# Kernel tuning notes

Measured on AMD Instinct MI355X. Metric: run time of the kernel, lower is better.

The kernel has to match this reference:

```python
import jax, jax.numpy as jnp
import numpy as np

N = 50000      # nodes
E = 800000     # edges (avg degree 16)
IN = 128       # in_channels
OUT = 64       # out_channels
HID = 2 * OUT  # 128, hidden width of conv1
EPS = 1e-5     # BatchNorm eps


def _edge_norm(edge_index):
    # PyG ChebConv with sym normalization, lambda_max=2: L_hat = -D^{-1/2} A D^{-1/2}
    src, dst = edge_index[0], edge_index[1]
    deg = jax.ops.segment_sum(jnp.ones((E,), jnp.float32), src, num_segments=N)
    dinv = jnp.where(deg > 0, jax.lax.rsqrt(jnp.maximum(deg, 1.0)), 0.0)
    return -dinv[src] * dinv[dst]


def _cheb(x, src, dst, norm, W0, W1, b):
    # K=2 Chebyshev conv: Tx0 = x, Tx1 = L_hat x (sparse propagate)
    tx1 = jax.ops.segment_sum(x[src] * norm[:, None], dst, num_segments=N)
    return x @ W0 + tx1 @ W1 + b


def setup_inputs() -> dict:
    key = jax.random.key(0)
    ks = jax.random.split(key, 14)
    g = lambda k, shp, fan: jax.random.normal(k, shp, jnp.float32) / np.sqrt(fan)
    return {
        "x": jax.random.normal(ks[0], (N, IN), jnp.float32),
        "edge_index": jax.random.randint(ks[1], (2, E), 0, N, dtype=jnp.int32),
        "W1_0": g(ks[2], (IN, HID), IN),
        "W1_1": g(ks[3], (IN, HID), IN),
        "b1": jnp.zeros((HID,), jnp.float32),
        "gamma": jnp.ones((HID,), jnp.float32),
        "beta": jnp.zeros((HID,), jnp.float32),
        "Wmu_0": g(ks[4], (HID, OUT), HID),
        "Wmu_1": g(ks[5], (HID, OUT), HID),
        "b_mu": jnp.zeros((OUT,), jnp.float32),
        "Wls_0": g(ks[6], (HID, OUT), HID),
        "Wls_1": g(ks[7], (HID, OUT), HID),
        "b_ls": jnp.zeros((OUT,), jnp.float32),
    }


def reference(x, edge_index, W1_0, W1_1, b1, gamma, beta,
              Wmu_0, Wmu_1, b_mu, Wls_0, Wls_1, b_ls):
    src, dst = edge_index[0], edge_index[1]
    norm = _edge_norm(edge_index)
    h = _cheb(x, src, dst, norm, W1_0, W1_1, b1)         # [N, HID]
    # BatchNorm1d (training mode: batch statistics over nodes)
    mean = jnp.mean(h, axis=0)
    var = jnp.var(h, axis=0)
    h = (h - mean) * jax.lax.rsqrt(var + EPS) * gamma + beta
    h = jax.nn.relu(h)
    mu = _cheb(h, src, dst, norm, Wmu_0, Wmu_1, b_mu)    # [N, OUT]
    logstd = _cheb(h, src, dst, norm, Wls_0, Wls_1, b_ls)
    return (mu, logstd)
```

## Files before the change

### kernel.cpp

```cpp
#include <hip/hip_runtime.h>
#include <cstddef>
#include <cstdint>

static constexpr int IN_C  = 128;
static constexpr float BN_EPS = 1e-5f;
static constexpr int OUT_C = 64;

static constexpr int CS_C = 32;
static constexpr int CS_R = 8;
static constexpr int CS_RANGE = 6250;

using bf16x8 = __attribute__((ext_vector_type(8))) short;
using f32x4  = __attribute__((ext_vector_type(4))) float;

__device__ __forceinline__ ushort f2bf(float f) {
    uint u = __float_as_uint(f);
    u += 0x7fffu + ((u >> 16) & 1u);
    return (ushort)(u >> 16);
}
__device__ __forceinline__ uint pack2(float a, float b) {
    return (uint)f2bf(a) | ((uint)f2bf(b) << 16);
}
__device__ __forceinline__ float bf_lo(uint v) { return __uint_as_float(v << 16); }
__device__ __forceinline__ float bf_hi(uint v) { return __uint_as_float(v & 0xffff0000u); }

__global__ __launch_bounds__(1024) void hist_k(
    const int* __restrict__ src, const int* __restrict__ dst,
    int* __restrict__ hsrc_part, int* __restrict__ hdst_part,
    int N, int E, int chunk, int range) {
    __shared__ int hs_[CS_RANGE];
    __shared__ int hd_[CS_RANGE];
    int c = blockIdx.x & (CS_C - 1);
    int r = blockIdx.x / CS_C;
    int base = r * range;
    int hi = min(base + range, N);
    int rsz = hi - base;
    for (int j = threadIdx.x; j < rsz; j += 1024) { hs_[j] = 0; hd_[j] = 0; }
    __syncthreads();
    int e0 = c * chunk, e1 = min(e0 + chunk, E);
    for (int i = e0 + threadIdx.x; i < e1; i += 1024) {
        int s = src[i];
        if (s >= base && s < hi) atomicAdd(&hs_[s - base], 1);
        int t = dst[i];
        if (t >= base && t < hi) atomicAdd(&hd_[t - base], 1);
    }
    __syncthreads();
    for (int j = threadIdx.x; j < rsz; j += 1024) {
        hsrc_part[(size_t)c * N + base + j] = hs_[j];
        hdst_part[(size_t)c * N + base + j] = hd_[j];
    }
}

__global__ void reduce_hist_k(const int* __restrict__ hsrc_part,
                              const int* __restrict__ hdst_part,
                              float* __restrict__ dinv, int* __restrict__ cnt_dst, int N) {
    int v = blockIdx.x * 256 + threadIdx.x;
    if (v >= N) return;
    int a = 0, b = 0;
    for (int c = 0; c < CS_C; ++c) {
        a += hsrc_part[(size_t)c * N + v];
        b += hdst_part[(size_t)c * N + v];
    }
    dinv[v] = (a > 0) ? rsqrtf((float)a) : 0.f;
    cnt_dst[v] = b;
}

__global__ void scan_reduce_k(const int* __restrict__ cnt, int* __restrict__ bsum, int n) {
    __shared__ int sw[16];
    int tid = threadIdx.x;
    int i0 = blockIdx.x * 4096 + tid * 4;
    int t = 0;
    if (i0 + 3 < n) {
        int4 c = *(const int4*)(cnt + i0);
        t = c.x + c.y + c.z + c.w;
    } else {
        #pragma unroll
        for (int j = 0; j < 4; ++j) if (i0 + j < n) t += cnt[i0 + j];
    }
    #pragma unroll
    for (int off = 1; off < 64; off <<= 1) t += __shfl_xor(t, off, 64);
    if ((tid & 63) == 0) sw[tid >> 6] = t;
    __syncthreads();
    if (tid == 0) {
        int a = 0;
        #pragma unroll
        for (int w = 0; w < 16; ++w) a += sw[w];
        bsum[blockIdx.x] = a;
    }
}

__global__ void scan_bsum_k(int* __restrict__ bsum, int nb) {
    int lane = threadIdx.x;
    int v = (lane < nb) ? bsum[lane] : 0;
    int s = v;
    #pragma unroll
    for (int off = 1; off < 64; off <<= 1) {
        int t = __shfl_up(s, off, 64);
        if (lane >= off) s += t;
    }
    if (lane < nb) bsum[lane] = s - v;
}

__global__ void scan_phase3_k(const int* __restrict__ cnt, const int* __restrict__ bsum,
                              int* __restrict__ row_ptr, int n) {
    __shared__ int sm_w[16];
    __shared__ int sm_excl[16];
    int tid = threadIdx.x;
    int lane = tid & 63, wid = tid >> 6;
    int base = blockIdx.x * 4096;
    int running = bsum[blockIdx.x];
    if (blockIdx.x == 0 && tid == 0) row_ptr[0] = 0;
    int i0 = base + tid * 4;
    int c0 = (i0     < n) ? cnt[i0]     : 0;
    int c1 = (i0 + 1 < n) ? cnt[i0 + 1] : 0;
    int c2 = (i0 + 2 < n) ? cnt[i0 + 2] : 0;
    int c3 = (i0 + 3 < n) ? cnt[i0 + 3] : 0;
    int tsum = c0 + c1 + c2 + c3;
    int s = tsum;
    #pragma unroll
    for (int off = 1; off < 64; off <<= 1) {
        int t = __shfl_up(s, off, 64);
        if (lane >= off) s += t;
    }
    if (lane == 63) sm_w[wid] = s;
    __syncthreads();
    if (tid == 0) {
        int acc = 0;
        #pragma unroll
        for (int w = 0; w < 16; ++w) { sm_excl[w] = acc; acc += sm_w[w]; }
    }
    __syncthreads();
    int excl = running + sm_excl[wid] + (s - tsum);
    if (i0     < n) row_ptr[i0 + 1] = excl + c0;
    if (i0 + 1 < n) row_ptr[i0 + 2] = excl + c0 + c1;
    if (i0 + 2 < n) row_ptr[i0 + 3] = excl + c0 + c1 + c2;
    if (i0 + 3 < n) row_ptr[i0 + 4] = excl + tsum;
}

__global__ void chunk_off_k(int* __restrict__ hdst_part, const int* __restrict__ row_ptr, int N) {
    int v = blockIdx.x * 256 + threadIdx.x;
    if (v >= N) return;
    int run = row_ptr[v];
    for (int c = 0; c < CS_C; ++c) {
        size_t idx = (size_t)c * N + v;
        int t = hdst_part[idx];
        hdst_part[idx] = run;
        run += t;
    }
}

__global__ __launch_bounds__(1024) void scatter_k(
    const int* __restrict__ src, const int* __restrict__ dst,
    const int* __restrict__ off, int* __restrict__ col,
    int N, int E, int chunk, int range) {
    __shared__ int cur[CS_RANGE];
    int c = blockIdx.x & (CS_C - 1);
    int r = blockIdx.x / CS_C;
    int base = r * range;
    int hi = min(base + range, N);
    int rsz = hi - base;
    for (int j = threadIdx.x; j < rsz; j += 1024)
        cur[j] = off[(size_t)c * N + base + j];
    __syncthreads();
    int e0 = c * chunk, e1 = min(e0 + chunk, E);
    for (int i = e0 + threadIdx.x; i < e1; i += 1024) {
        int t = dst[i];
        if (t >= base && t < hi) {
            int pos = atomicAdd(&cur[t - base], 1);
            col[pos] = src[i];
        }
    }
}

__global__ void convert_x_k(const float* __restrict__ in, const float* __restrict__ dinv,
                            ushort* __restrict__ xb, ushort* __restrict__ xsb, int n64) {
    int i = blockIdx.x * blockDim.x + threadIdx.x;
    if (i >= n64) return;
    int row = i >> 6;
    float d = dinv[row];
    float2 v = ((const float2*)in)[i];
    ((uint*)xb)[i] = pack2(v.x, v.y);
    ((uint*)xsb)[i] = pack2(v.x * d, v.y * d);
}

__global__ void prep_weights_k(const float* __restrict__ W1_0, const float* __restrict__ W1_1,
                               const float* __restrict__ b1,
                               const float* __restrict__ Wmu_0, const float* __restrict__ Wmu_1,
                               const float* __restrict__ b_mu,
                               const float* __restrict__ Wls_0, const float* __restrict__ Wls_1,
                               const float* __restrict__ b_ls,
                               ushort* __restrict__ Wt1, ushort* __restrict__ Wt2,
                               float* __restrict__ bias1, float* __restrict__ bias2) {
    int idx = blockIdx.x * blockDim.x + threadIdx.x;
    int which = idx >> 15;
    int c = (idx >> 8) & 127;
    int k = idx & 255;
    if (which == 0) {
        float v = (k < 128) ? W1_0[k * 128 + c] : W1_1[(k - 128) * 128 + c];
        Wt1[c * 256 + k] = f2bf(v);
        if (k == 0) bias1[c] = b1[c];
    } else {
        float v;
        if (c < 64) v = (k < 128) ? Wmu_0[k * 64 + c] : Wmu_1[(k - 128) * 64 + c];
        else        v = (k < 128) ? Wls_0[k * 64 + (c - 64)] : Wls_1[(k - 128) * 64 + (c - 64)];
        Wt2[c * 256 + k] = f2bf(v);
        if (k == 0) bias2[c] = (c < 64) ? b_mu[c] : b_ls[c - 64];
    }
}

#define ACC8(V)                                         \
    acc[0] += bf_lo((V).x); acc[1] += bf_hi((V).x);     \
    acc[2] += bf_lo((V).y); acc[3] += bf_hi((V).y);     \
    acc[4] += bf_lo((V).z); acc[5] += bf_hi((V).z);     \
    acc[6] += bf_lo((V).w); acc[7] += bf_hi((V).w);

__global__ __launch_bounds__(256) void propagate4_k(
    const uint4* __restrict__ xs, uint4* __restrict__ out,
    const int* __restrict__ row_ptr, const int* __restrict__ col,
    const float* __restrict__ dinv, int n) {
    int wid = (blockIdx.x * 256 + threadIdx.x) >> 6;
    if (wid >= n) return;
    int lane = threadIdx.x & 63;
    int g = lane >> 4, li = lane & 15;
    int s = row_ptr[wid], e = row_ptr[wid + 1];
    float acc[8];
    #pragma unroll
    for (int k = 0; k < 8; ++k) acc[k] = 0.f;
    int i = s + g;
    for (; i + 12 < e; i += 16) {
        int c0 = col[i];
        int c1 = col[i + 4];
        int c2 = col[i + 8];
        int c3 = col[i + 12];
        uint4 v0 = xs[(size_t)c0 * 16 + li];
        uint4 v1 = xs[(size_t)c1 * 16 + li];
        uint4 v2 = xs[(size_t)c2 * 16 + li];
        uint4 v3 = xs[(size_t)c3 * 16 + li];
        ACC8(v0); ACC8(v1); ACC8(v2); ACC8(v3);
    }
    for (; i < e; i += 4) {
        int c0 = col[i];
        uint4 v0 = xs[(size_t)c0 * 16 + li];
        ACC8(v0);
    }
    #pragma unroll
    for (int k = 0; k < 8; ++k) {
        acc[k] += __shfl_xor(acc[k], 16, 64);
        acc[k] += __shfl_xor(acc[k], 32, 64);
    }
    if (g == 0) {
        float sc = -dinv[wid];
        uint4 o;
        o.x = pack2(acc[0] * sc, acc[1] * sc);
        o.y = pack2(acc[2] * sc, acc[3] * sc);
        o.z = pack2(acc[4] * sc, acc[5] * sc);
        o.w = pack2(acc[6] * sc, acc[7] * sc);
        out[(size_t)wid * 16 + li] = o;
    }
}

template <int MODE>
__global__ __launch_bounds__(256) void gemm_mfma_k(
    const ushort* __restrict__ A0, const ushort* __restrict__ A1,
    const ushort* __restrict__ Wt, const float* __restrict__ bias,
    ushort* __restrict__ Cb, float* __restrict__ Cmu, float* __restrict__ Cls, int n) {
    __shared__ ushort sA[64][32];
    __shared__ ushort sW[128][32];

    int tid = threadIdx.x;
    int block_row = blockIdx.x * 64;
    int wave = tid >> 6, lane = tid & 63;
    int m_local = wave * 16 + (lane & 15);
    int quad = lane >> 4;

    f32x4 acc[8];
    #pragma unroll
    for (int t = 0; t < 8; ++t) acc[t] = (f32x4){0.f, 0.f, 0.f, 0.f};

    for (int k0 = 0; k0 < 256; k0 += 32) {
        {
            int row = tid >> 2, koff = (tid & 3) * 8;
            int grow = block_row + row;
            int kc = k0 + koff;
            uint4 v = make_uint4(0, 0, 0, 0);
            if (grow < n) {
                const ushort* srcp = (kc < 128) ? (A0 + (size_t)grow * 128 + kc)
                                                : (A1 + (size_t)grow * 128 + (kc - 128));
                v = *(const uint4*)srcp;
            }
            *(uint4*)&sA[row][koff] = v;
        }
        #pragma unroll
        for (int i = tid; i < 512; i += 256) {
            int c = i >> 2, koff = (i & 3) * 8;
            *(uint4*)&sW[c][koff] = *(const uint4*)(Wt + (size_t)c * 256 + k0 + koff);
        }
        __syncthreads();
        bf16x8 af = *(const bf16x8*)&sA[m_local][quad * 8];
        #pragma unroll
        for (int t = 0; t < 8; ++t) {
            bf16x8 bfr = *(const bf16x8*)&sW[t * 16 + (lane & 15)][quad * 8];
            acc[t] = __builtin_amdgcn_mfma_f32_16x16x32_bf16(af, bfr, acc[t], 0, 0, 0);
        }
        __syncthreads();
    }

    int col_base = lane & 15;
    int row_l = wave * 16 + quad * 4;
    #pragma unroll
    for (int t = 0; t < 8; ++t) {
        int col = t * 16 + col_base;
        float b = bias[col];
        #pragma unroll
        for (int r = 0; r < 4; ++r) {
            int grow = block_row + row_l + r;
            if (grow < n) {
                float v = acc[t][r] + b;
                if (MODE == 0) {
                    Cb[(size_t)grow * 128 + col] = f2bf(v);
                } else {
                    if (col < 64) Cmu[(size_t)grow * 64 + col] = v;
                    else          Cls[(size_t)grow * 64 + (col - 64)] = v;
                }
            }
        }
    }
}

__global__ __launch_bounds__(256) void bn_stats_k(const ushort* __restrict__ hb,
                                                  float* __restrict__ stats, int n) {
    __shared__ float sm[1024];
    int tid = threadIdx.x;
    int p = tid & 63;
    int rw = tid >> 6;
    float s0 = 0.f, q0 = 0.f, s1 = 0.f, q1 = 0.f;
    for (int r = blockIdx.x * 4 + rw; r < n; r += gridDim.x * 4) {
        uint v = ((const uint*)hb)[(size_t)r * 64 + p];
        float f0 = bf_lo(v), f1 = bf_hi(v);
        s0 += f0; q0 += f0 * f0;
        s1 += f1; q1 += f1 * f1;
    }
    sm[tid] = s0; sm[256 + tid] = q0; sm[512 + tid] = s1; sm[768 + tid] = q1;
    __syncthreads();
    if (tid < 64) {
        #pragma unroll
        for (int q = 0; q < 4; ++q) {
            float v = sm[q * 256 + tid] + sm[q * 256 + tid + 64] +
                      sm[q * 256 + tid + 128] + sm[q * 256 + tid + 192];
            int col = 2 * tid + (q >> 1);
            atomicAdd(&stats[col + ((q & 1) ? 128 : 0)], v);
        }
    }
}

__global__ void bn_finalize_k(const float* __restrict__ stats, const float* __restrict__ gamma,
                              const float* __restrict__ beta, float* __restrict__ p, float inv_n) {
    int c = threadIdx.x;
    float mean = stats[c] * inv_n;
    float var = stats[128 + c] * inv_n - mean * mean;
    float sc = gamma[c] * rsqrtf(var + BN_EPS);
    p[c] = sc;
    p[128 + c] = beta[c] - mean * sc;
}

__global__ void bn_apply_relu_bf_k(ushort* __restrict__ hb, ushort* __restrict__ hsb,
                                   const float* __restrict__ p, const float* __restrict__ dinv,
                                   int n64) {
    int i = blockIdx.x * blockDim.x + threadIdx.x;
    if (i >= n64) return;
    int c2 = (i & 63) * 2;
    int row = i >> 6;
    uint v = ((uint*)hb)[i];
    float f0 = fmaxf(bf_lo(v) * p[c2]     + p[128 + c2],     0.f);
    float f1 = fmaxf(bf_hi(v) * p[c2 + 1] + p[128 + c2 + 1], 0.f);
    ((uint*)hb)[i] = pack2(f0, f1);
    float d = dinv[row];
    ((uint*)hsb)[i] = pack2(f0 * d, f1 * d);
}

extern "C" void kernel_launch(void* const* d_in, const int* in_sizes, int n_in,
                              void* d_out, int out_size, void* d_ws, size_t ws_size,
                              hipStream_t stream) {
    const float* x = (const float*)d_in[0];
    const int* edge_index = (const int*)d_in[1];
    const float* W1_0 = (const float*)d_in[2];
    const float* W1_1 = (const float*)d_in[3];
    const float* b1 = (const float*)d_in[4];
    const float* gamma = (const float*)d_in[5];
    const float* beta = (const float*)d_in[6];
    const float* Wmu_0 = (const float*)d_in[7];
    const float* Wmu_1 = (const float*)d_in[8];
    const float* b_mu = (const float*)d_in[9];
    const float* Wls_0 = (const float*)d_in[10];
    const float* Wls_1 = (const float*)d_in[11];
    const float* b_ls = (const float*)d_in[12];

    const int N = in_sizes[0] / IN_C;
    const int E = in_sizes[1] / 2;
    const int* src = edge_index;
    const int* dst = edge_index + E;

    char* w = (char*)d_ws;
    auto alloc = [&](size_t bytes) {
        char* p = w;
        w += (bytes + 15) & ~(size_t)15;
        return p;
    };
    float* stats = (float*)alloc(256 * 4);
    size_t zero_bytes = (size_t)(w - (char*)stats);
    int* row_ptr = (int*)alloc((size_t)(N + 1) * 4);
    int* bsum    = (int*)alloc(64 * 4);
    float* dinv  = (float*)alloc((size_t)N * 4);
    int* cnt_dst = (int*)alloc((size_t)N * 4);
    int* col     = (int*)alloc((size_t)E * 4);
    int* hsrc_part = (int*)alloc((size_t)CS_C * N * 4);
    int* hdst_part = (int*)alloc((size_t)CS_C * N * 4);
    float* bnp   = (float*)alloc(256 * 4);
    ushort* x_bf  = (ushort*)alloc((size_t)N * 128 * 2);
    ushort* xs_bf = (ushort*)alloc((size_t)N * 128 * 2);
    ushort* xp_bf = (ushort*)alloc((size_t)N * 128 * 2);
    ushort* h_bf  = (ushort*)alloc((size_t)N * 128 * 2);
    ushort* Wt1   = (ushort*)alloc(128 * 256 * 2);
    ushort* Wt2   = (ushort*)alloc(128 * 256 * 2);
    float* bias1  = (float*)alloc(128 * 4);
    float* bias2  = (float*)alloc(128 * 4);

    ushort* hs_bf = xs_bf;
    ushort* hp_bf = xp_bf;

    float* out_mu = (float*)d_out;
    float* out_ls = out_mu + (size_t)N * OUT_C;

    hipMemsetAsync(stats, 0, zero_bytes, stream);

    int chunk = (E + CS_C - 1) / CS_C;
    int range = (N + CS_R - 1) / CS_R;
    int NB = (N + 4095) / 4096;

    hist_k<<<CS_R * CS_C, 1024, 0, stream>>>(src, dst, hsrc_part, hdst_part, N, E, chunk, range);
    reduce_hist_k<<<(N + 255) / 256, 256, 0, stream>>>(hsrc_part, hdst_part, dinv, cnt_dst, N);

    scan_reduce_k<<<NB, 1024, 0, stream>>>(cnt_dst, bsum, N);
    scan_bsum_k<<<1, 64, 0, stream>>>(bsum, NB);
    scan_phase3_k<<<NB, 1024, 0, stream>>>(cnt_dst, bsum, row_ptr, N);

    chunk_off_k<<<(N + 255) / 256, 256, 0, stream>>>(hdst_part, row_ptr, N);
    scatter_k<<<CS_R * CS_C, 1024, 0, stream>>>(src, dst, hdst_part, col, N, E, chunk, range);

    convert_x_k<<<(N * 64 + 255) / 256, 256, 0, stream>>>(x, dinv, x_bf, xs_bf, N * 64);
    prep_weights_k<<<256, 256, 0, stream>>>(W1_0, W1_1, b1, Wmu_0, Wmu_1, b_mu,
                                            Wls_0, Wls_1, b_ls, Wt1, Wt2, bias1, bias2);

    int pb = (N + 3) / 4;
    propagate4_k<<<pb, 256, 0, stream>>>((const uint4*)xs_bf, (uint4*)xp_bf,
                                         row_ptr, col, dinv, N);

    int gb = (N + 63) / 64;
    gemm_mfma_k<0><<<gb, 256, 0, stream>>>(x_bf, xp_bf, Wt1, bias1, h_bf, nullptr, nullptr, N);

    bn_stats_k<<<256, 256, 0, stream>>>(h_bf, stats, N);
    bn_finalize_k<<<1, 128, 0, stream>>>(stats, gamma, beta, bnp, 1.f / (float)N);
    bn_apply_relu_bf_k<<<(N * 64 + 255) / 256, 256, 0, stream>>>(h_bf, hs_bf, bnp, dinv, N * 64);

    propagate4_k<<<pb, 256, 0, stream>>>((const uint4*)hs_bf, (uint4*)hp_bf,
                                         row_ptr, col, dinv, N);

    gemm_mfma_k<1><<<gb, 256, 0, stream>>>(h_bf, hp_bf, Wt2, bias2, nullptr, out_mu, out_ls, N);
}
```

Measured before the change: 310.2 us.

## Fuse preprocessing kernels, drop memset and bn finalize, widen GEMM tile

Several small launches are merged. Histogram reduction is combined with the block-sum step, and the scan's final phase is combined with the per-chunk offset computation, which now uses int4 accesses. Input conversion is merged with weight prep, and BN finalize moves into the apply kernel. The stats memset is replaced by a zeroing write inside count_k, and each GEMM block now covers 128 rows with two accumulator sets. This removes roughly six launches and their gaps, but each phase3 block sums bsum serially, and the larger GEMM tile raises register use and halves the block count.

```diff
diff --git a/kernel.cpp b/kernel.cpp
--- a/kernel.cpp
+++ b/kernel.cpp
@@ -51,35 +51,32 @@
     }
 }
 
-__global__ void reduce_hist_k(const int* __restrict__ hsrc_part,
-                              const int* __restrict__ hdst_part,
-                              float* __restrict__ dinv, int* __restrict__ cnt_dst, int N) {
-    int v = blockIdx.x * 256 + threadIdx.x;
-    if (v >= N) return;
-    int a = 0, b = 0;
-    for (int c = 0; c < CS_C; ++c) {
-        a += hsrc_part[(size_t)c * N + v];
-        b += hdst_part[(size_t)c * N + v];
-    }
-    dinv[v] = (a > 0) ? rsqrtf((float)a) : 0.f;
-    cnt_dst[v] = b;
-}
-
-__global__ void scan_reduce_k(const int* __restrict__ cnt, int* __restrict__ bsum, int n) {
+__global__ __launch_bounds__(1024) void count_k(
+    const int* __restrict__ hsrc_part, const int* __restrict__ hdst_part,
+    float* __restrict__ dinv, int* __restrict__ cnt_dst,
+    int* __restrict__ bsum, float* __restrict__ stats, int N) {
     __shared__ int sw[16];
     int tid = threadIdx.x;
-    int i0 = blockIdx.x * 4096 + tid * 4;
-    int t = 0;
-    if (i0 + 3 < n) {
-        int4 c = *(const int4*)(cnt + i0);
-        t = c.x + c.y + c.z + c.w;
-    } else {
-        #pragma unroll
-        for (int j = 0; j < 4; ++j) if (i0 + j < n) t += cnt[i0 + j];
-    }
-    #pragma unroll
-    for (int off = 1; off < 64; off <<= 1) t += __shfl_xor(t, off, 64);
-    if ((tid & 63) == 0) sw[tid >> 6] = t;
+    if (blockIdx.x == 0 && tid < 256) stats[tid] = 0.f;
+    int base = blockIdx.x * 4096;
+    int tsum = 0;
+    #pragma unroll
+    for (int j = 0; j < 4; ++j) {
+        int v = base + j * 1024 + tid;
+        if (v < N) {
+            int a = 0, b = 0;
+            for (int c = 0; c < CS_C; ++c) {
+                a += hsrc_part[(size_t)c * N + v];
+                b += hdst_part[(size_t)c * N + v];
+            }
+            dinv[v] = (a > 0) ? rsqrtf((float)a) : 0.f;
+            cnt_dst[v] = b;
+            tsum += b;
+        }
+    }
+    #pragma unroll
+    for (int off = 1; off < 64; off <<= 1) tsum += __shfl_xor(tsum, off, 64);
+    if ((tid & 63) == 0) sw[tid >> 6] = tsum;
     __syncthreads();
     if (tid == 0) {
         int a = 0;
@@ -89,27 +86,21 @@
     }
 }
 
-__global__ void scan_bsum_k(int* __restrict__ bsum, int nb) {
-    int lane = threadIdx.x;
-    int v = (lane < nb) ? bsum[lane] : 0;
-    int s = v;
-    #pragma unroll
-    for (int off = 1; off < 64; off <<= 1) {
-        int t = __shfl_up(s, off, 64);
-        if (lane >= off) s += t;
-    }
-    if (lane < nb) bsum[lane] = s - v;
-}
-
-__global__ void scan_phase3_k(const int* __restrict__ cnt, const int* __restrict__ bsum,
-                              int* __restrict__ row_ptr, int n) {
+__global__ __launch_bounds__(1024) void phase3_k(
+    const int* __restrict__ cnt, const int* __restrict__ bsum,
+    int* __restrict__ row_ptr, int* __restrict__ hdst_part, int n, int nb) {
     __shared__ int sm_w[16];
     __shared__ int sm_excl[16];
+    __shared__ int sm_base;
     int tid = threadIdx.x;
     int lane = tid & 63, wid = tid >> 6;
     int base = blockIdx.x * 4096;
-    int running = bsum[blockIdx.x];
-    if (blockIdx.x == 0 && tid == 0) row_ptr[0] = 0;
+    if (tid == 0) {
+        int run = 0;
+        for (int b = 0; b < (int)blockIdx.x; ++b) run += bsum[b];
+        sm_base = run;
+        if (blockIdx.x == 0) row_ptr[0] = 0;
+    }
     int i0 = base + tid * 4;
     int c0 = (i0     < n) ? cnt[i0]     : 0;
     int c1 = (i0 + 1 < n) ? cnt[i0 + 1] : 0;
@@ -130,22 +121,25 @@
         for (int w = 0; w < 16; ++w) { sm_excl[w] = acc; acc += sm_w[w]; }
     }
     __syncthreads();
-    int excl = running + sm_excl[wid] + (s - tsum);
-    if (i0     < n) row_ptr[i0 + 1] = excl + c0;
-    if (i0 + 1 < n) row_ptr[i0 + 2] = excl + c0 + c1;
-    if (i0 + 2 < n) row_ptr[i0 + 3] = excl + c0 + c1 + c2;
+    int excl = sm_base + sm_excl[wid] + (s - tsum);
+    int st0 = excl, st1 = excl + c0, st2 = st1 + c1, st3 = st2 + c2;
+    if (i0     < n) row_ptr[i0 + 1] = st1;
+    if (i0 + 1 < n) row_ptr[i0 + 2] = st2;
+    if (i0 + 2 < n) row_ptr[i0 + 3] = st3;
     if (i0 + 3 < n) row_ptr[i0 + 4] = excl + tsum;
-}
-
-__global__ void chunk_off_k(int* __restrict__ hdst_part, const int* __restrict__ row_ptr, int N) {
-    int v = blockIdx.x * 256 + threadIdx.x;
-    if (v >= N) return;
-    int run = row_ptr[v];
+    int r0 = st0, r1 = st1, r2 = st2, r3 = st3;
     for (int c = 0; c < CS_C; ++c) {
-        size_t idx = (size_t)c * N + v;
-        int t = hdst_part[idx];
-        hdst_part[idx] = run;
-        run += t;
+        size_t idx = (size_t)c * n + i0;
+        if (i0 + 3 < n) {
+            int4 t = *(const int4*)(hdst_part + idx);
+            int4 o = make_int4(r0, r1, r2, r3);
+            *(int4*)(hdst_part + idx) = o;
+            r0 += t.x; r1 += t.y; r2 += t.z; r3 += t.w;
+        } else {
+            if (i0 < n)     { int t = hdst_part[idx];     hdst_part[idx] = r0;     r0 += t; }
+            if (i0 + 1 < n) { int t = hdst_part[idx + 1]; hdst_part[idx + 1] = r1; r1 += t; }
+            if (i0 + 2 < n) { int t = hdst_part[idx + 2]; hdst_part[idx + 2] = r2; r2 += t; }
+        }
     }
 }
 
@@ -172,18 +166,10 @@
     }
 }
 
-__global__ void convert_x_k(const float* __restrict__ in, const float* __restrict__ dinv,
-                            ushort* __restrict__ xb, ushort* __restrict__ xsb, int n64) {
-    int i = blockIdx.x * blockDim.x + threadIdx.x;
-    if (i >= n64) return;
-    int row = i >> 6;
-    float d = dinv[row];
-    float2 v = ((const float2*)in)[i];
-    ((uint*)xb)[i] = pack2(v.x, v.y);
-    ((uint*)xsb)[i] = pack2(v.x * d, v.y * d);
-}
-
-__global__ void prep_weights_k(const float* __restrict__ W1_0, const float* __restrict__ W1_1,
+__global__ void convert_prep_k(const float* __restrict__ in, const float* __restrict__ dinv,
+                               ushort* __restrict__ xb, ushort* __restrict__ xsb, int n64,
+                               int nb_conv,
+                               const float* __restrict__ W1_0, const float* __restrict__ W1_1,
                                const float* __restrict__ b1,
                                const float* __restrict__ Wmu_0, const float* __restrict__ Wmu_1,
                                const float* __restrict__ b_mu,
@@ -191,20 +177,31 @@
                                const float* __restrict__ b_ls,
                                ushort* __restrict__ Wt1, ushort* __restrict__ Wt2,
                                float* __restrict__ bias1, float* __restrict__ bias2) {
-    int idx = blockIdx.x * blockDim.x + threadIdx.x;
-    int which = idx >> 15;
-    int c = (idx >> 8) & 127;
-    int k = idx & 255;
-    if (which == 0) {
-        float v = (k < 128) ? W1_0[k * 128 + c] : W1_1[(k - 128) * 128 + c];
-        Wt1[c * 256 + k] = f2bf(v);
-        if (k == 0) bias1[c] = b1[c];
+    int bid = blockIdx.x;
+    if (bid < nb_conv) {
+        int i = bid * 256 + threadIdx.x;
+        if (i >= n64) return;
+        int row = i >> 6;
+        float d = dinv[row];
+        float2 v = ((const float2*)in)[i];
+        ((uint*)xb)[i] = pack2(v.x, v.y);
+        ((uint*)xsb)[i] = pack2(v.x * d, v.y * d);
     } else {
-        float v;
-        if (c < 64) v = (k < 128) ? Wmu_0[k * 64 + c] : Wmu_1[(k - 128) * 64 + c];
-        else        v = (k < 128) ? Wls_0[k * 64 + (c - 64)] : Wls_1[(k - 128) * 64 + (c - 64)];
-        Wt2[c * 256 + k] = f2bf(v);
-        if (k == 0) bias2[c] = (c < 64) ? b_mu[c] : b_ls[c - 64];
+        int idx = (bid - nb_conv) * 256 + threadIdx.x;
+        int which = idx >> 15;
+        int c = (idx >> 8) & 127;
+        int k = idx & 255;
+        if (which == 0) {
+            float v = (k < 128) ? W1_0[k * 128 + c] : W1_1[(k - 128) * 128 + c];
+            Wt1[c * 256 + k] = f2bf(v);
+            if (k == 0) bias1[c] = b1[c];
+        } else {
+            float v;
+            if (c < 64) v = (k < 128) ? Wmu_0[k * 64 + c] : Wmu_1[(k - 128) * 64 + c];
+            else        v = (k < 128) ? Wls_0[k * 64 + (c - 64)] : Wls_1[(k - 128) * 64 + (c - 64)];
+            Wt2[c * 256 + k] = f2bf(v);
+            if (k == 0) bias2[c] = (c < 64) ? b_mu[c] : b_ls[c - 64];
+        }
     }
 }
 
@@ -264,22 +261,29 @@
     const ushort* __restrict__ A0, const ushort* __restrict__ A1,
     const ushort* __restrict__ Wt, const float* __restrict__ bias,
     ushort* __restrict__ Cb, float* __restrict__ Cmu, float* __restrict__ Cls, int n) {
-    __shared__ ushort sA[64][32];
+    __shared__ ushort sA[128][32];
     __shared__ ushort sW[128][32];
 
     int tid = threadIdx.x;
-    int block_row = blockIdx.x * 64;
+    int block_row = blockIdx.x * 128;
     int wave = tid >> 6, lane = tid & 63;
-    int m_local = wave * 16 + (lane & 15);
+    int col_base = lane & 15;
     int quad = lane >> 4;
-
-    f32x4 acc[8];
-    #pragma unroll
-    for (int t = 0; t < 8; ++t) acc[t] = (f32x4){0.f, 0.f, 0.f, 0.f};
+    int m0 = wave * 32 + col_base;
+    int m1 = m0 + 16;
+
+    f32x4 acc0[8], acc1[8];
+    #pragma unroll
+    for (int t = 0; t < 8; ++t) {
+        acc0[t] = (f32x4){0.f, 0.f, 0.f, 0.f};
+        acc1[t] = (f32x4){0.f, 0.f, 0.f, 0.f};
+    }
 
     for (int k0 = 0; k0 < 256; k0 += 32) {
-        {
-            int row = tid >> 2, koff = (tid & 3) * 8;
+        #pragma unroll
+        for (int p = 0; p < 2; ++p) {
+            int row = (tid >> 2) + p * 64;
+            int koff = (tid & 3) * 8;
             int grow = block_row + row;
             int kc = k0 + koff;
             uint4 v = make_uint4(0, 0, 0, 0);
@@ -296,32 +300,37 @@
             *(uint4*)&sW[c][koff] = *(const uint4*)(Wt + (size_t)c * 256 + k0 + koff);
         }
         __syncthreads();
-        bf16x8 af = *(const bf16x8*)&sA[m_local][quad * 8];
+        bf16x8 a0 = *(const bf16x8*)&sA[m0][quad * 8];
+        bf16x8 a1 = *(const bf16x8*)&sA[m1][quad * 8];
         #pragma unroll
         for (int t = 0; t < 8; ++t) {
-            bf16x8 bfr = *(const bf16x8*)&sW[t * 16 + (lane & 15)][quad * 8];
-            acc[t] = __builtin_amdgcn_mfma_f32_16x16x32_bf16(af, bfr, acc[t], 0, 0, 0);
+            bf16x8 bfr = *(const bf16x8*)&sW[t * 16 + col_base][quad * 8];
+            acc0[t] = __builtin_amdgcn_mfma_f32_16x16x32_bf16(a0, bfr, acc0[t], 0, 0, 0);
+            acc1[t] = __builtin_amdgcn_mfma_f32_16x16x32_bf16(a1, bfr, acc1[t], 0, 0, 0);
         }
         __syncthreads();
     }
 
-    int col_base = lane & 15;
-    int row_l = wave * 16 + quad * 4;
+    int row_l0 = wave * 32 + quad * 4;
     #pragma unroll
     for (int t = 0; t < 8; ++t) {
         int col = t * 16 + col_base;
         float b = bias[col];
         #pragma unroll
         for (int r = 0; r < 4; ++r) {
-            int grow = block_row + row_l + r;
-            if (grow < n) {
-                float v = acc[t][r] + b;
-                if (MODE == 0) {
-                    Cb[(size_t)grow * 128 + col] = f2bf(v);
-                } else {
-                    if (col < 64) Cmu[(size_t)grow * 64 + col] = v;
-                    else          Cls[(size_t)grow * 64 + (col - 64)] = v;
-                }
+            int g0 = block_row + row_l0 + r;
+            int g1 = g0 + 16;
+            if (g0 < n) {
+                float v = acc0[t][r] + b;
+                if (MODE == 0) Cb[(size_t)g0 * 128 + col] = f2bf(v);
+                else if (col < 64) Cmu[(size_t)g0 * 64 + col] = v;
+                else               Cls[(size_t)g0 * 64 + (col - 64)] = v;
+            }
+            if (g1 < n) {
+                float v = acc1[t][r] + b;
+                if (MODE == 0) Cb[(size_t)g1 * 128 + col] = f2bf(v);
+                else if (col < 64) Cmu[(size_t)g1 * 64 + col] = v;
+                else               Cls[(size_t)g1 * 64 + (col - 64)] = v;
             }
         }
     }
@@ -353,26 +362,28 @@
     }
 }
 
-__global__ void bn_finalize_k(const float* __restrict__ stats, const float* __restrict__ gamma,
-                              const float* __restrict__ beta, float* __restrict__ p, float inv_n) {
-    int c = threadIdx.x;
-    float mean = stats[c] * inv_n;
-    float var = stats[128 + c] * inv_n - mean * mean;
-    float sc = gamma[c] * rsqrtf(var + BN_EPS);
-    p[c] = sc;
-    p[128 + c] = beta[c] - mean * sc;
-}
-
-__global__ void bn_apply_relu_bf_k(ushort* __restrict__ hb, ushort* __restrict__ hsb,
-                                   const float* __restrict__ p, const float* __restrict__ dinv,
-                                   int n64) {
-    int i = blockIdx.x * blockDim.x + threadIdx.x;
+__global__ __launch_bounds__(256) void bn_apply_k(
+    ushort* __restrict__ hb, ushort* __restrict__ hsb,
+    const float* __restrict__ stats, const float* __restrict__ gamma,
+    const float* __restrict__ beta, const float* __restrict__ dinv,
+    float inv_n, int n64) {
+    __shared__ float sp[256];
+    int tid = threadIdx.x;
+    if (tid < 128) {
+        float mean = stats[tid] * inv_n;
+        float var = stats[128 + tid] * inv_n - mean * mean;
+        float sc = gamma[tid] * rsqrtf(var + BN_EPS);
+        sp[tid] = sc;
+        sp[128 + tid] = beta[tid] - mean * sc;
+    }
+    __syncthreads();
+    int i = blockIdx.x * 256 + tid;
     if (i >= n64) return;
     int c2 = (i & 63) * 2;
     int row = i >> 6;
     uint v = ((uint*)hb)[i];
-    float f0 = fmaxf(bf_lo(v) * p[c2]     + p[128 + c2],     0.f);
-    float f1 = fmaxf(bf_hi(v) * p[c2 + 1] + p[128 + c2 + 1], 0.f);
+    float f0 = fmaxf(bf_lo(v) * sp[c2]     + sp[128 + c2],     0.f);
+    float f1 = fmaxf(bf_hi(v) * sp[c2 + 1] + sp[128 + c2 + 1], 0.f);
     ((uint*)hb)[i] = pack2(f0, f1);
     float d = dinv[row];
     ((uint*)hsb)[i] = pack2(f0 * d, f1 * d);
@@ -407,7 +418,6 @@
         return p;
     };
     float* stats = (float*)alloc(256 * 4);
-    size_t zero_bytes = (size_t)(w - (char*)stats);
     int* row_ptr = (int*)alloc((size_t)(N + 1) * 4);
     int* bsum    = (int*)alloc(64 * 4);
     float* dinv  = (float*)alloc((size_t)N * 4);
@@ -415,7 +425,6 @@
     int* col     = (int*)alloc((size_t)E * 4);
     int* hsrc_part = (int*)alloc((size_t)CS_C * N * 4);
     int* hdst_part = (int*)alloc((size_t)CS_C * N * 4);
-    float* bnp   = (float*)alloc(256 * 4);
     ushort* x_bf  = (ushort*)alloc((size_t)N * 128 * 2);
     ushort* xs_bf = (ushort*)alloc((size_t)N * 128 * 2);
     ushort* xp_bf = (ushort*)alloc((size_t)N * 128 * 2);
@@ -431,36 +440,31 @@
     float* out_mu = (float*)d_out;
     float* out_ls = out_mu + (size_t)N * OUT_C;
 
-    hipMemsetAsync(stats, 0, zero_bytes, stream);
-
     int chunk = (E + CS_C - 1) / CS_C;
     int range = (N + CS_R - 1) / CS_R;
     int NB = (N + 4095) / 4096;
+    int nb_conv = (N * 64 + 255) / 256;
 
     hist_k<<<CS_R * CS_C, 1024, 0, stream>>>(src, dst, hsrc_part, hdst_part, N, E, chunk, range);
-    reduce_hist_k<<<(N + 255) / 256, 256, 0, stream>>>(hsrc_part, hdst_part, dinv, cnt_dst, N);
-
-    scan_reduce_k<<<NB, 1024, 0, stream>>>(cnt_dst, bsum, N);
-    scan_bsum_k<<<1, 64, 0, stream>>>(bsum, NB);
-    scan_phase3_k<<<NB, 1024, 0, stream>>>(cnt_dst, bsum, row_ptr, N);
-
-    chunk_off_k<<<(N + 255) / 256, 256, 0, stream>>>(hdst_part, row_ptr, N);
+    count_k<<<NB, 1024, 0, stream>>>(hsrc_part, hdst_part, dinv, cnt_dst, bsum, stats, N);
+    phase3_k<<<NB, 1024, 0, stream>>>(cnt_dst, bsum, row_ptr, hdst_part, N, NB);
     scatter_k<<<CS_R * CS_C, 1024, 0, stream>>>(src, dst, hdst_part, col, N, E, chunk, range);
 
-    convert_x_k<<<(N * 64 + 255) / 256, 256, 0, stream>>>(x, dinv, x_bf, xs_bf, N * 64);
-    prep_weights_k<<<256, 256, 0, stream>>>(W1_0, W1_1, b1, Wmu_0, Wmu_1, b_mu,
-                                            Wls_0, Wls_1, b_ls, Wt1, Wt2, bias1, bias2);
+    convert_prep_k<<<nb_conv + 256, 256, 0, stream>>>(
+        x, dinv, x_bf, xs_bf, N * 64, nb_conv,
+        W1_0, W1_1, b1, Wmu_0, Wmu_1, b_mu, Wls_0, Wls_1, b_ls,
+        Wt1, Wt2, bias1, bias2);
 
     int pb = (N + 3) / 4;
     propagate4_k<<<pb, 256, 0, stream>>>((const uint4*)xs_bf, (uint4*)xp_bf,
                                          row_ptr, col, dinv, N);
 
-    int gb = (N + 63) / 64;
+    int gb = (N + 127) / 128;
     gemm_mfma_k<0><<<gb, 256, 0, stream>>>(x_bf, xp_bf, Wt1, bias1, h_bf, nullptr, nullptr, N);
 
     bn_stats_k<<<256, 256, 0, stream>>>(h_bf, stats, N);
-    bn_finalize_k<<<1, 128, 0, stream>>>(stats, gamma, beta, bnp, 1.f / (float)N);
-    bn_apply_relu_bf_k<<<(N * 64 + 255) / 256, 256, 0, stream>>>(h_bf, hs_bf, bnp, dinv, N * 64);
+    bn_apply_k<<<(N * 64 + 255) / 256, 256, 0, stream>>>(h_bf, hs_bf, stats, gamma, beta,
+                                                         dinv, 1.f / (float)N, N * 64);
 
     propagate4_k<<<pb, 256, 0, stream>>>((const uint4*)hs_bf, (uint4*)hp_bf,
                                          row_ptr, col, dinv, N);
```

New measurement: 320.3 us. 1.03x slower.
